# Kernel tuning notes

Hardware: AMD Instinct MI355X
Metric: run time of the kernel (lower is better)

The kernel has to match this reference:

```python
import jax, jax.numpy as jnp
import numpy as np

BATCH, IN_F, OUT_F = 1024, 512, 512
GRID_SIZE, SPLINE_ORDER = 32, 3
P_DEACTIVATE = 0.1


def b_splines(x, grid, k):
    """x: (n, in), grid: (in, G+2k+1) -> bases (n, in, G+k). Cox-de Boor recursion."""
    x = x[..., None]  # (n, in, 1)
    bases = ((x >= grid[:, :-1]) & (x < grid[:, 1:])).astype(x.dtype)
    for j in range(1, k + 1):
        left = (x - grid[:, : -(j + 1)]) / (grid[:, j:-1] - grid[:, : -(j + 1)])
        right = (grid[:, j + 1:] - x) / (grid[:, j + 1:] - grid[:, 1:-j])
        bases = left * bases[..., :-1] + right * bases[..., 1:]
    return bases


def setup_inputs() -> dict:
    key = jax.random.key(0)
    k1, k2, k3, k4, k5 = jax.random.split(key, 5)
    # uniform extended grid over [-1, 1], same for every input feature
    h = 2.0 / GRID_SIZE
    knots = np.arange(-SPLINE_ORDER, GRID_SIZE + SPLINE_ORDER + 1, dtype=np.float32) * h - 1.0
    grid = jnp.asarray(np.tile(knots, (IN_F, 1)))  # (in, G+2k+1)
    return {
        "x": jax.random.normal(k1, (BATCH, IN_F), jnp.float32),
        "base_weight": jax.random.normal(k2, (OUT_F, IN_F), jnp.float32) * 0.05,
        "spline_weight": jax.random.normal(k3, (OUT_F, IN_F, GRID_SIZE + SPLINE_ORDER), jnp.float32) * 0.1,
        "spline_scaler": jax.random.normal(k4, (OUT_F, IN_F), jnp.float32),
        "grid": grid,
        "deactivate_mask": jax.random.bernoulli(k5, P_DEACTIVATE, (OUT_F, IN_F)),
    }


def reference(x, base_weight, spline_weight, spline_scaler, grid, deactivate_mask):
    k = SPLINE_ORDER
    weights = spline_weight * spline_scaler[..., None]  # scaled_spline_weight (o, i, c)
    # base path: F.linear(silu(x), base_weight)
    base_out = jax.nn.silu(x) @ base_weight.T  # (b, o)
    # spline path
    bases = b_splines(x, grid, k)  # (b, i, c)
    contrib = jnp.einsum('bic,oic->boi', bases, weights)  # (b, o, i)
    # linear fallback from spline values at grid endpoints
    gmin = grid[:, k].min()
    gmax = grid[:, -k - 1].max()
    ends_x = jnp.stack([gmin, gmax])[:, None] * jnp.ones((1, x.shape[1]), x.dtype)  # (2, i)
    y_ends = jnp.einsum('nic,oic->noi', b_splines(ends_x, grid, k), weights)  # (2, o, i)
    y_start, y_end = y_ends[0], y_ends[1]
    dx = gmax - gmin
    degenerate = jnp.abs(dx) < 1e-8
    a = jnp.where(degenerate, 0.0, (y_end - y_start) / jnp.where(degenerate, 1.0, dx))  # (o, i)
    b = y_start - a * gmin
    lin = a[None] * x[:, None, :] + b[None]  # (b, o, i)
    final = jnp.where(deactivate_mask[None], lin, contrib)
    return base_out + final.sum(axis=2)
```

## Files before the change

kernel.cpp:

```cpp
#include <hip/hip_runtime.h>
#include <hip/hip_bf16.h>


typedef unsigned short u16;
typedef unsigned int u32;
typedef unsigned long long u64;
typedef __attribute__((ext_vector_type(8))) short short8;
typedef __attribute__((ext_vector_type(4))) float floatx4;
typedef __attribute__((ext_vector_type(4))) unsigned int uintx4;

#define IN_F 512
#define OUT_F 512
#define BATCH 1024
#define K_SPLINE (IN_F * 36)
#define K_BASE_OFF K_SPLINE
#define K_LIN_OFF (K_SPLINE + IN_F)
#define K_TOT (K_SPLINE + 2 * IN_F)
#define SPLITS 32
#define MN (BATCH * OUT_F)

static __device__ inline u16 f2b(float f) {
  union { float f; u32 u; } v; v.f = f;
  u32 r = v.u + 0x7FFFu + ((v.u >> 16) & 1u);
  return (u16)(r >> 16);
}
static __device__ inline float b2f(u32 lo16) {
  union { u32 u; float f; } v; v.u = lo16 << 16; return v.f;
}

__global__ __launch_bounds__(256) void prep_kernel(
    const float* __restrict__ bw, const float* __restrict__ sw,
    const float* __restrict__ sc, const void* __restrict__ maskp,
    const float* __restrict__ x, u16* __restrict__ B,
    float* __restrict__ bias_part, u64* __restrict__ PB8) {
  __shared__ u64 lds64[1120 * 4];
  __shared__ int sflag;
  __shared__ float ws4[4];
  int blk = blockIdx.x, t = threadIdx.x;

  if (blk >= 1024) {
    int id = (blk - 1024) * 256 + t;
    float xv = x[id];
    int mc = (int)floorf((xv + 1.1875f) * 16.0f);
    float gm = (float)mc * 0.0625f - 1.1875f;
    if (xv < gm) { mc -= 1; gm -= 0.0625f; }
    else if (xv >= gm + 0.0625f) { mc += 1; gm += 0.0625f; }
    u32 lo, hi;
    if (mc >= 0 && mc <= 37) {
      float t_ = (xv - gm) * 16.0f;
      float t2 = t_ * t_, t3 = t2 * t_;
      float omt = 1.0f - t_;
      u16 r0 = f2b(omt * omt * omt * (1.0f / 6.0f));
      u16 r1 = f2b((3.0f * t3 - 6.0f * t2 + 4.0f) * (1.0f / 6.0f));
      u16 r2 = f2b((-3.0f * t3 + 3.0f * t2 + 3.0f * t_ + 1.0f) * (1.0f / 6.0f));
      lo = (u32)r0 | ((u32)r1 << 16);
      hi = (u32)r2 | ((u32)mc << 16);
    } else {
      lo = 0; hi = 0xFFFF0000u;
    }
    PB8[id] = (u64)lo | ((u64)hi << 32);
    return;
  }

  float* lds_f = (float*)lds64;
  u16* lds_u = (u16*)lds64;
  int id = blk * 256 + t;
  int o = id >> 9, i = id & 511;
  int i0 = (blk & 1) * 256;

  const float* swb = sw + ((size_t)o * 512 + i0) * 35;
#pragma unroll
  for (int j = 0; j < 35; ++j) lds_f[j * 256 + t] = swb[j * 256 + t];

  const u32* mw = (const u32*)maskp;
  if (t == 0) sflag = 0;
  __syncthreads();
  if (t < 64) {
    u32 w2 = mw[blk * 64 + t];
    if ((w2 & 0xFFFFFF00u) && w2 != 0x3F800000u) atomicOr(&sflag, 1);
  }
  __syncthreads();
  int fl = sflag;
  if (!(fl & 1)) {
    u32 w1 = mw[blk * 256 + t];
    if (w1 == 0x3F800000u) atomicOr(&sflag, 2);
  }
  __syncthreads();
  fl = sflag;
  bool mk;
  if (fl & 1)      mk = ((const unsigned char*)maskp)[id] != 0;
  else if (fl & 2) mk = ((const float*)maskp)[id] != 0.0f;
  else             mk = ((const int*)maskp)[id] != 0;

  float s = sc[id];
  float w[35];
#pragma unroll
  for (int c = 0; c < 35; ++c) w[c] = lds_f[t * 35 + c] * s;
  __syncthreads();

  float ys = (w[0] + 4.0f * w[1] + w[2]) * (1.0f / 6.0f);
  float ye = (w[32] + 4.0f * w[33] + w[34]) * (1.0f / 6.0f);
  float a = (ye - ys) * 0.5f;
  float bl = ys + a;

#pragma unroll
  for (int c = 0; c < 35; ++c) lds_u[t * 36 + c] = f2b(mk ? 0.0f : w[c]);
  lds_u[t * 36 + 35] = 0;

  B[(size_t)o * K_TOT + K_BASE_OFF + i] = f2b(bw[id]);
  B[(size_t)o * K_TOT + K_LIN_OFF + i] = f2b(mk ? a : 0.0f);

  float v = mk ? bl : 0.0f;
#pragma unroll
  for (int off = 32; off >= 1; off >>= 1) v += __shfl_down(v, off);
  if ((t & 63) == 0) ws4[t >> 6] = v;
  __syncthreads();
  if (t == 0) bias_part[blk] = ws4[0] + ws4[1] + ws4[2] + ws4[3];

  u64* dst = (u64*)(B + (size_t)o * K_TOT + (size_t)i0 * 36);
#pragma unroll
  for (int j = 0; j < 9; ++j) dst[j * 256 + t] = lds64[j * 256 + t];
}

__global__ __launch_bounds__(256, 4) void gemm_fused(const float* __restrict__ x,
                                                     const u64* __restrict__ PB8,
                                                     const u16* __restrict__ Bp,
                                                     u16* __restrict__ P) {
  __shared__ u16 As[128 * 64 + 64];
  __shared__ u16 Bs[128 * 64];

  int t = threadIdx.x;
  int id = blockIdx.x;
  int ks = id >> 5, tile = id & 31;
  int bm = tile >> 2, bn = tile & 3;
  int w = t >> 6, l = t & 63;
  int wm = w & 1, wn = w >> 1;

  floatx4 acc[4][4];
#pragma unroll
  for (int p = 0; p < 4; ++p)
#pragma unroll
    for (int q = 0; q < 4; ++q) acc[p][q] = (floatx4)0.0f;

  int nit = (ks < 16) ? 10 : 9;
  int k0s = (ks < 16) ? ks * 640 : 10240 + (ks - 16) * 576;

  int ra = t >> 3;
  int cg = (t & 7) ^ (ra & 7);
  const u16* Bg = Bp + (size_t)(bn * 128 + ra) * K_TOT + k0s + cg * 8;
  u16* Bsp = Bs + t * 8;

  int rr_ = t >> 1, hf = t & 1;
  int rx7 = rr_ & 7;
  int dummy = 128 * 64 + (t & 63);
  const u64* PBrow = PB8 + (size_t)(bm * 128 + rr_) * IN_F;

  int mr = l & 15;
  int cq = l >> 4;

  int if_cur = 0; u64 e0 = 0, e1 = 0;
  if (k0s < K_BASE_OFF) {
    if_cur = (k0s + hf * 32) / 36;
    e0 = PBrow[if_cur];
    e1 = PBrow[if_cur + 1];
  }

  int k0 = k0s;
  for (int kk = 0; kk < nit; ++kk, k0 += 64) {
#pragma unroll
    for (int p = 0; p < 4; ++p)
      __builtin_amdgcn_global_load_lds(
          (const __attribute__((address_space(1))) void*)(Bg + (size_t)p * 32 * K_TOT),
          (__attribute__((address_space(3))) void*)(Bsp + p * 2048), 16, 0, 0);
    Bg += 64;

    int if_nxt = if_cur; u64 en0 = e0, en1 = e1;
    if (k0 < K_BASE_OFF) {
#pragma unroll
      for (int q = 0; q < 4; ++q) {
        int ch = hf * 4 + q;
        *(uintx4*)&As[rr_ * 64 + ((ch ^ rx7) << 3)] = (uintx4)0u;
      }
      int k0w = k0 + hf * 32;
      int i_last = (k0w + 31) / 36;
#pragma unroll
      for (int ii = 0; ii < 2; ++ii) {
        int i = if_cur + ii;
        if (i <= i_last) {
          u64 e = ii ? e1 : e0;
          u32 lo = (u32)e, hi = (u32)(e >> 32);
          int mc = (int)(hi >> 16);
          float f0 = b2f(lo & 0xFFFFu);
          float f1 = b2f(lo >> 16);
          float f2 = b2f(hi & 0xFFFFu);
          u16 bv[4] = {(u16)lo, (u16)(lo >> 16), (u16)hi, f2b(1.0f - f0 - f1 - f2)};
          int cb = i * 36 + mc - 3 - k0;
#pragma unroll
          for (int j = 0; j < 4; ++j) {
            int c = cb + j;
            bool ok = ((u32)(c - hf * 32) < 32u) && ((u32)(mc - 3 + j) < 35u);
            int addr = ok ? (rr_ * 64 + (((c >> 3) ^ rx7) << 3) + (c & 7)) : dummy;
            As[addr] = bv[j];
          }
        }
      }
      int k0n = k0 + 64;
      if (k0n < K_BASE_OFF) {
        if_nxt = (k0n + hf * 32) / 36;
        en0 = PBrow[if_nxt];
        en1 = PBrow[if_nxt + 1];
      }
    } else {
      bool isBase = (k0 < K_LIN_OFF);
      int xb = isBase ? (k0 - K_BASE_OFF) : (k0 - K_LIN_OFF);
#pragma unroll
      for (int p = 0; p < 4; ++p) {
        int cid = t + 256 * p;
        int row = cid >> 3, ch = cid & 7;
        const float* xp = &x[(size_t)(bm * 128 + row) * IN_F + xb + ch * 8];
        floatx4 v0 = *(const floatx4*)xp;
        floatx4 v1 = *(const floatx4*)(xp + 4);
        float f[8] = {v0.x, v0.y, v0.z, v0.w, v1.x, v1.y, v1.z, v1.w};
        u16 r[8];
#pragma unroll
        for (int j = 0; j < 8; ++j) {
          float vv = f[j];
          if (isBase) vv = vv / (1.0f + __expf(-vv));
          r[j] = f2b(vv);
        }
        *(short8*)(As + row * 64 + ((ch ^ (row & 7)) << 3)) = *(short8*)r;
      }
    }
    __syncthreads();

#pragma unroll
    for (int h = 0; h < 2; ++h) {
      short8 af[4], bf[4];
      int c = h * 4 + cq;
#pragma unroll
      for (int tm = 0; tm < 4; ++tm) {
        int row = wm * 64 + tm * 16 + mr;
        af[tm] = *(const short8*)&As[row * 64 + ((c ^ (row & 7)) << 3)];
      }
#pragma unroll
      for (int tn = 0; tn < 4; ++tn) {
        int row = wn * 64 + tn * 16 + mr;
        bf[tn] = *(const short8*)&Bs[row * 64 + ((c ^ (row & 7)) << 3)];
      }
#pragma unroll
      for (int tm = 0; tm < 4; ++tm)
#pragma unroll
        for (int tn = 0; tn < 4; ++tn)
          acc[tm][tn] = __builtin_amdgcn_mfma_f32_16x16x32_bf16(af[tm], bf[tn], acc[tm][tn], 0, 0, 0);
    }
    __syncthreads();
    if_cur = if_nxt; e0 = en0; e1 = en1;
  }

  u16* Pb = P + ((size_t)tile * SPLITS + ks) * 16384;
#pragma unroll
  for (int q = 0; q < 8; ++q) {
    int tm = q >> 1, tn0 = (q & 1) * 2;
    u16 r[8];
#pragma unroll
    for (int z = 0; z < 4; ++z) r[z] = f2b(acc[tm][tn0][z]);
#pragma unroll
    for (int z = 0; z < 4; ++z) r[4 + z] = f2b(acc[tm][tn0 + 1][z]);
    *(short8*)(Pb + q * 2048 + t * 8) = *(short8*)r;
  }
}

__global__ __launch_bounds__(256) void reduce_kernel(const u16* __restrict__ P,
                                                     const float* __restrict__ bias_part,
                                                     float* __restrict__ out) {
  int rid = blockIdx.x * 256 + threadIdx.x;
  int tile = rid >> 11;
  int rem = rid & 2047;
  int q = rem >> 8, t = rem & 255;
  const u16* base = P + (size_t)tile * SPLITS * 16384 + q * 2048 + t * 8;

  float s[8] = {0, 0, 0, 0, 0, 0, 0, 0};
#pragma unroll
  for (int ks = 0; ks < SPLITS; ++ks) {
    short8 v = *(const short8*)(base + (size_t)ks * 16384);
#pragma unroll
    for (int j = 0; j < 8; ++j) s[j] += b2f((u32)(u16)v[j]);
  }

  int w = t >> 6, l = t & 63;
  int wm = w & 1, wn = w >> 1;
  int bm = tile >> 2, bn = tile & 3;
  int row0 = bm * 128 + wm * 64 + ((l >> 4) << 2);
  int col0 = bn * 128 + wn * 64 + (l & 15);
  int tm = q >> 1, tn0 = (q & 1) * 2;
#pragma unroll
  for (int j = 0; j < 8; ++j) {
    int tn = tn0 + (j >> 2), rr = j & 3;
    int row = row0 + tm * 16 + rr;
    int col = col0 + tn * 16;
    float bsv = bias_part[2 * col] + bias_part[2 * col + 1];
    out[(size_t)row * OUT_F + col] = s[j] + bsv;
  }
}

extern "C" void kernel_launch(void* const* d_in, const int* in_sizes, int n_in,
                              void* d_out, int out_size, void* d_ws, size_t ws_size,
                              hipStream_t stream) {
  const float* x  = (const float*)d_in[0];
  const float* bw = (const float*)d_in[1];
  const float* sw = (const float*)d_in[2];
  const float* sc = (const float*)d_in[3];
  const void* mask = d_in[5];

  const size_t B_BYTES = (size_t)OUT_F * K_TOT * 2;
  const size_t BIAS_OFF = B_BYTES;
  const size_t PB_OFF = B_BYTES + 8192;
  const size_t PB_BYTES = (size_t)MN * 8;
  const size_t P_OFF = PB_OFF + PB_BYTES;

  char* wsb = (char*)d_ws;
  u16* Bpack = (u16*)wsb;
  float* bias_part = (float*)(wsb + BIAS_OFF);
  u64* PB8 = (u64*)(wsb + PB_OFF);
  u16* P = (u16*)(wsb + P_OFF);

  prep_kernel<<<3072, 256, 0, stream>>>(bw, sw, sc, mask, x, Bpack, bias_part, PB8);
  gemm_fused<<<1024, 256, 0, stream>>>(x, PB8, Bpack, P);
  reduce_kernel<<<256, 256, 0, stream>>>(P, bias_part, (float*)d_out);
}
```

Before: 138.2 us.

## Double-buffer LDS tiles in GEMM and halve split-K count

The GEMM now keeps two LDS buffers for A and B. It issues the next tile's global-to-LDS B load and builds the next A tile while MFMAs consume the current buffers, which leaves one barrier per iteration. Split-K drops from 32 to 16 equal chunks of 19 iterations each, so half as many blocks launch and half as many partials reach the reduce step. LDS per block doubles and occupancy is lowered to 2 blocks per CU. The prep kernel also copies spline weights into LDS with 16-byte vector loads.

```diff
diff --git a/kernel.cpp b/kernel.cpp
--- a/kernel.cpp
+++ b/kernel.cpp
@@ -16,7 +16,9 @@
 #define K_BASE_OFF K_SPLINE
 #define K_LIN_OFF (K_SPLINE + IN_F)
 #define K_TOT (K_SPLINE + 2 * IN_F)
-#define SPLITS 32
+#define SPLITS 16
+#define KPS 1216
+#define NIT 19
 #define MN (BATCH * OUT_F)
 
 static __device__ inline u16 f2b(float f) {
@@ -33,7 +35,7 @@
     const float* __restrict__ sc, const void* __restrict__ maskp,
     const float* __restrict__ x, u16* __restrict__ B,
     float* __restrict__ bias_part, u64* __restrict__ PB8) {
-  __shared__ u64 lds64[1120 * 4];
+  __shared__ __align__(16) u64 lds64[1120 * 4];
   __shared__ int sflag;
   __shared__ float ws4[4];
   int blk = blockIdx.x, t = threadIdx.x;
@@ -69,8 +71,11 @@
   int i0 = (blk & 1) * 256;
 
   const float* swb = sw + ((size_t)o * 512 + i0) * 35;
-#pragma unroll
-  for (int j = 0; j < 35; ++j) lds_f[j * 256 + t] = swb[j * 256 + t];
+  const floatx4* sw4 = (const floatx4*)swb;
+  floatx4* lds4 = (floatx4*)lds_f;
+#pragma unroll
+  for (int j = 0; j < 8; ++j) lds4[j * 256 + t] = sw4[j * 256 + t];
+  if (t < 192) lds4[8 * 256 + t] = sw4[8 * 256 + t];
 
   const u32* mw = (const u32*)maskp;
   if (t == 0) sflag = 0;
@@ -122,12 +127,12 @@
   for (int j = 0; j < 9; ++j) dst[j * 256 + t] = lds64[j * 256 + t];
 }
 
-__global__ __launch_bounds__(256, 4) void gemm_fused(const float* __restrict__ x,
+__global__ __launch_bounds__(256, 2) void gemm_fused(const float* __restrict__ x,
                                                      const u64* __restrict__ PB8,
                                                      const u16* __restrict__ Bp,
                                                      u16* __restrict__ P) {
-  __shared__ u16 As[128 * 64 + 64];
-  __shared__ u16 Bs[128 * 64];
+  __shared__ u16 As[2][128 * 64 + 64];
+  __shared__ u16 Bs[2][128 * 64];
 
   int t = threadIdx.x;
   int id = blockIdx.x;
@@ -142,13 +147,11 @@
 #pragma unroll
     for (int q = 0; q < 4; ++q) acc[p][q] = (floatx4)0.0f;
 
-  int nit = (ks < 16) ? 10 : 9;
-  int k0s = (ks < 16) ? ks * 640 : 10240 + (ks - 16) * 576;
+  int k0s = ks * KPS;
 
   int ra = t >> 3;
   int cg = (t & 7) ^ (ra & 7);
-  const u16* Bg = Bp + (size_t)(bn * 128 + ra) * K_TOT + k0s + cg * 8;
-  u16* Bsp = Bs + t * 8;
+  const u16* Bgp = Bp + (size_t)(bn * 128 + ra) * K_TOT + k0s + cg * 8;
 
   int rr_ = t >> 1, hf = t & 1;
   int rx7 = rr_ & 7;
@@ -158,34 +161,27 @@
   int mr = l & 15;
   int cq = l >> 4;
 
-  int if_cur = 0; u64 e0 = 0, e1 = 0;
-  if (k0s < K_BASE_OFF) {
-    if_cur = (k0s + hf * 32) / 36;
-    e0 = PBrow[if_cur];
-    e1 = PBrow[if_cur + 1];
-  }
-
-  int k0 = k0s;
-  for (int kk = 0; kk < nit; ++kk, k0 += 64) {
-#pragma unroll
-    for (int p = 0; p < 4; ++p)
-      __builtin_amdgcn_global_load_lds(
-          (const __attribute__((address_space(1))) void*)(Bg + (size_t)p * 32 * K_TOT),
-          (__attribute__((address_space(3))) void*)(Bsp + p * 2048), 16, 0, 0);
-    Bg += 64;
-
-    int if_nxt = if_cur; u64 en0 = e0, en1 = e1;
-    if (k0 < K_BASE_OFF) {
+  int if_c = 0; u64 e0 = 0, e1 = 0;
+  auto load_PB = [&](int k0b) {
+    if (k0b < K_BASE_OFF) {
+      if_c = (k0b + hf * 32) / 36;
+      e0 = PBrow[if_c];
+      e1 = PBrow[if_c + 1];
+    }
+  };
+
+  auto build_A = [&](int k0b, u16* Asb) {
+    if (k0b < K_BASE_OFF) {
 #pragma unroll
       for (int q = 0; q < 4; ++q) {
         int ch = hf * 4 + q;
-        *(uintx4*)&As[rr_ * 64 + ((ch ^ rx7) << 3)] = (uintx4)0u;
-      }
-      int k0w = k0 + hf * 32;
+        *(uintx4*)&Asb[rr_ * 64 + ((ch ^ rx7) << 3)] = (uintx4)0u;
+      }
+      int k0w = k0b + hf * 32;
       int i_last = (k0w + 31) / 36;
 #pragma unroll
       for (int ii = 0; ii < 2; ++ii) {
-        int i = if_cur + ii;
+        int i = if_c + ii;
         if (i <= i_last) {
           u64 e = ii ? e1 : e0;
           u32 lo = (u32)e, hi = (u32)(e >> 32);
@@ -194,25 +190,19 @@
           float f1 = b2f(lo >> 16);
           float f2 = b2f(hi & 0xFFFFu);
           u16 bv[4] = {(u16)lo, (u16)(lo >> 16), (u16)hi, f2b(1.0f - f0 - f1 - f2)};
-          int cb = i * 36 + mc - 3 - k0;
+          int cb = i * 36 + mc - 3 - k0b;
 #pragma unroll
           for (int j = 0; j < 4; ++j) {
             int c = cb + j;
             bool ok = ((u32)(c - hf * 32) < 32u) && ((u32)(mc - 3 + j) < 35u);
             int addr = ok ? (rr_ * 64 + (((c >> 3) ^ rx7) << 3) + (c & 7)) : dummy;
-            As[addr] = bv[j];
+            Asb[addr] = bv[j];
           }
         }
       }
-      int k0n = k0 + 64;
-      if (k0n < K_BASE_OFF) {
-        if_nxt = (k0n + hf * 32) / 36;
-        en0 = PBrow[if_nxt];
-        en1 = PBrow[if_nxt + 1];
-      }
     } else {
-      bool isBase = (k0 < K_LIN_OFF);
-      int xb = isBase ? (k0 - K_BASE_OFF) : (k0 - K_LIN_OFF);
+      bool isBase = (k0b < K_LIN_OFF);
+      int xb = isBase ? (k0b - K_BASE_OFF) : (k0b - K_LIN_OFF);
 #pragma unroll
       for (int p = 0; p < 4; ++p) {
         int cid = t + 256 * p;
@@ -228,11 +218,43 @@
           if (isBase) vv = vv / (1.0f + __expf(-vv));
           r[j] = f2b(vv);
         }
-        *(short8*)(As + row * 64 + ((ch ^ (row & 7)) << 3)) = *(short8*)r;
-      }
-    }
-    __syncthreads();
-
+        *(short8*)(Asb + row * 64 + ((ch ^ (row & 7)) << 3)) = *(short8*)r;
+      }
+    }
+  };
+
+  {
+    u16* Bsp = &Bs[0][t * 8];
+#pragma unroll
+    for (int p = 0; p < 4; ++p)
+      __builtin_amdgcn_global_load_lds(
+          (const __attribute__((address_space(1))) void*)(Bgp + (size_t)p * 32 * K_TOT),
+          (__attribute__((address_space(3))) void*)(Bsp + p * 2048), 16, 0, 0);
+    Bgp += 64;
+    load_PB(k0s);
+    build_A(k0s, &As[0][0]);
+    load_PB(k0s + 64);
+  }
+  __syncthreads();
+
+  int k0 = k0s;
+#pragma unroll 2
+  for (int kk = 0; kk < NIT; ++kk, k0 += 64) {
+    int cur = kk & 1, nxt = cur ^ 1;
+    if (kk + 1 < NIT) {
+      u16* Bsp = &Bs[nxt][t * 8];
+#pragma unroll
+      for (int p = 0; p < 4; ++p)
+        __builtin_amdgcn_global_load_lds(
+            (const __attribute__((address_space(1))) void*)(Bgp + (size_t)p * 32 * K_TOT),
+            (__attribute__((address_space(3))) void*)(Bsp + p * 2048), 16, 0, 0);
+      Bgp += 64;
+      build_A(k0 + 64, &As[nxt][0]);
+      if (kk + 2 < NIT) load_PB(k0 + 128);
+    }
+
+    const u16* Ac = &As[cur][0];
+    const u16* Bc = &Bs[cur][0];
 #pragma unroll
     for (int h = 0; h < 2; ++h) {
       short8 af[4], bf[4];
@@ -240,12 +262,12 @@
 #pragma unroll
       for (int tm = 0; tm < 4; ++tm) {
         int row = wm * 64 + tm * 16 + mr;
-        af[tm] = *(const short8*)&As[row * 64 + ((c ^ (row & 7)) << 3)];
+        af[tm] = *(const short8*)&Ac[row * 64 + ((c ^ (row & 7)) << 3)];
       }
 #pragma unroll
       for (int tn = 0; tn < 4; ++tn) {
         int row = wn * 64 + tn * 16 + mr;
-        bf[tn] = *(const short8*)&Bs[row * 64 + ((c ^ (row & 7)) << 3)];
+        bf[tn] = *(const short8*)&Bc[row * 64 + ((c ^ (row & 7)) << 3)];
       }
 #pragma unroll
       for (int tm = 0; tm < 4; ++tm)
@@ -254,7 +276,6 @@
           acc[tm][tn] = __builtin_amdgcn_mfma_f32_16x16x32_bf16(af[tm], bf[tn], acc[tm][tn], 0, 0, 0);
     }
     __syncthreads();
-    if_cur = if_nxt; e0 = en0; e1 = en1;
   }
 
   u16* Pb = P + ((size_t)tile * SPLITS + ks) * 16384;
@@ -325,6 +346,6 @@
   u16* P = (u16*)(wsb + P_OFF);
 
   prep_kernel<<<3072, 256, 0, stream>>>(bw, sw, sc, mask, x, Bpack, bias_part, PB8);
-  gemm_fused<<<1024, 256, 0, stream>>>(x, PB8, Bpack, P);
+  gemm_fused<<<512, 256, 0, stream>>>(x, PB8, Bpack, P);
   reduce_kernel<<<256, 256, 0, stream>>>(P, bias_part, (float*)d_out);
 }
```

Result: slower. 147.2 us (+6.5%).

## Materialize dense bf16 A matrix in prep and stream it via global_load_lds

Applied to the files above, without the earlier changes.

The prep kernel now writes a fully dense bf16 A operand (spline bases, silu(x) and x per batch row) to workspace, replacing the compact 4-nonzero encoding. The GEMM loads both A and B tiles directly into LDS with async global_load_lds and no longer builds A tiles from packed entries. This removes per-iteration scatter, zeroing and silu work from the GEMM inner loop. In exchange it writes and reads about 38 MB of mostly-zero A data through memory. The spline-weight staging copy in prep is also widened to 16-byte vector loads.

```diff
diff --git a/kernel.cpp b/kernel.cpp
--- a/kernel.cpp
+++ b/kernel.cpp
@@ -7,7 +7,6 @@
 typedef unsigned long long u64;
 typedef __attribute__((ext_vector_type(8))) short short8;
 typedef __attribute__((ext_vector_type(4))) float floatx4;
-typedef __attribute__((ext_vector_type(4))) unsigned int uintx4;
 
 #define IN_F 512
 #define OUT_F 512
@@ -32,20 +31,27 @@
     const float* __restrict__ bw, const float* __restrict__ sw,
     const float* __restrict__ sc, const void* __restrict__ maskp,
     const float* __restrict__ x, u16* __restrict__ B,
-    float* __restrict__ bias_part, u64* __restrict__ PB8) {
-  __shared__ u64 lds64[1120 * 4];
+    float* __restrict__ bias_part, u16* __restrict__ A) {
+  __shared__ __align__(16) u64 lds64[1120 * 4];
   __shared__ int sflag;
   __shared__ float ws4[4];
   int blk = blockIdx.x, t = threadIdx.x;
 
   if (blk >= 1024) {
-    int id = (blk - 1024) * 256 + t;
-    float xv = x[id];
+    int bix = blk - 1024;
+    int b = bix >> 1;
+    int i0 = (bix & 1) << 8;
+    int i = i0 + t;
+    float xv = x[(size_t)b * IN_F + i];
+
+    u64* myrow = lds64 + t * 9;
+#pragma unroll
+    for (int j = 0; j < 9; ++j) myrow[j] = 0;
+
     int mc = (int)floorf((xv + 1.1875f) * 16.0f);
     float gm = (float)mc * 0.0625f - 1.1875f;
     if (xv < gm) { mc -= 1; gm -= 0.0625f; }
     else if (xv >= gm + 0.0625f) { mc += 1; gm += 0.0625f; }
-    u32 lo, hi;
     if (mc >= 0 && mc <= 37) {
       float t_ = (xv - gm) * 16.0f;
       float t2 = t_ * t_, t3 = t2 * t_;
@@ -53,12 +59,24 @@
       u16 r0 = f2b(omt * omt * omt * (1.0f / 6.0f));
       u16 r1 = f2b((3.0f * t3 - 6.0f * t2 + 4.0f) * (1.0f / 6.0f));
       u16 r2 = f2b((-3.0f * t3 + 3.0f * t2 + 3.0f * t_ + 1.0f) * (1.0f / 6.0f));
-      lo = (u32)r0 | ((u32)r1 << 16);
-      hi = (u32)r2 | ((u32)mc << 16);
-    } else {
-      lo = 0; hi = 0xFFFF0000u;
+      float f0 = b2f(r0), f1 = b2f(r1), f2 = b2f(r2);
+      u16 bv[4] = {r0, r1, r2, f2b(1.0f - f0 - f1 - f2)};
+      u16* lds_u = (u16*)lds64;
+#pragma unroll
+      for (int j = 0; j < 4; ++j) {
+        int c = mc - 3 + j;
+        if ((u32)c < 35u) lds_u[t * 36 + c] = bv[j];
+      }
     }
-    PB8[id] = (u64)lo | ((u64)hi << 32);
+    __syncthreads();
+
+    u64* dstA = (u64*)(A + (size_t)b * K_TOT + (size_t)i0 * 36);
+#pragma unroll
+    for (int j = 0; j < 9; ++j) dstA[j * 256 + t] = lds64[j * 256 + t];
+
+    float sl = xv / (1.0f + __expf(-xv));
+    A[(size_t)b * K_TOT + K_BASE_OFF + i] = f2b(sl);
+    A[(size_t)b * K_TOT + K_LIN_OFF + i] = f2b(xv);
     return;
   }
 
@@ -69,8 +87,11 @@
   int i0 = (blk & 1) * 256;
 
   const float* swb = sw + ((size_t)o * 512 + i0) * 35;
-#pragma unroll
-  for (int j = 0; j < 35; ++j) lds_f[j * 256 + t] = swb[j * 256 + t];
+  const floatx4* sw4 = (const floatx4*)swb;
+  floatx4* lds4 = (floatx4*)lds_f;
+#pragma unroll
+  for (int j = 0; j < 8; ++j) lds4[j * 256 + t] = sw4[j * 256 + t];
+  if (t < 192) lds4[8 * 256 + t] = sw4[8 * 256 + t];
 
   const u32* mw = (const u32*)maskp;
   if (t == 0) sflag = 0;
@@ -122,11 +143,10 @@
   for (int j = 0; j < 9; ++j) dst[j * 256 + t] = lds64[j * 256 + t];
 }
 
-__global__ __launch_bounds__(256, 4) void gemm_fused(const float* __restrict__ x,
-                                                     const u64* __restrict__ PB8,
+__global__ __launch_bounds__(256, 4) void gemm_fused(const u16* __restrict__ A,
                                                      const u16* __restrict__ Bp,
                                                      u16* __restrict__ P) {
-  __shared__ u16 As[128 * 64 + 64];
+  __shared__ u16 As[128 * 64];
   __shared__ u16 Bs[128 * 64];
 
   int t = threadIdx.x;
@@ -147,90 +167,27 @@
 
   int ra = t >> 3;
   int cg = (t & 7) ^ (ra & 7);
-  const u16* Bg = Bp + (size_t)(bn * 128 + ra) * K_TOT + k0s + cg * 8;
+  const u16* Agp = A + (size_t)(bm * 128 + ra) * K_TOT + k0s + cg * 8;
+  const u16* Bgp = Bp + (size_t)(bn * 128 + ra) * K_TOT + k0s + cg * 8;
+  u16* Asp = As + t * 8;
   u16* Bsp = Bs + t * 8;
-
-  int rr_ = t >> 1, hf = t & 1;
-  int rx7 = rr_ & 7;
-  int dummy = 128 * 64 + (t & 63);
-  const u64* PBrow = PB8 + (size_t)(bm * 128 + rr_) * IN_F;
 
   int mr = l & 15;
   int cq = l >> 4;
 
-  int if_cur = 0; u64 e0 = 0, e1 = 0;
-  if (k0s < K_BASE_OFF) {
-    if_cur = (k0s + hf * 32) / 36;
-    e0 = PBrow[if_cur];
-    e1 = PBrow[if_cur + 1];
-  }
-
-  int k0 = k0s;
-  for (int kk = 0; kk < nit; ++kk, k0 += 64) {
+  for (int kk = 0; kk < nit; ++kk) {
 #pragma unroll
     for (int p = 0; p < 4; ++p)
       __builtin_amdgcn_global_load_lds(
-          (const __attribute__((address_space(1))) void*)(Bg + (size_t)p * 32 * K_TOT),
+          (const __attribute__((address_space(1))) void*)(Agp + (size_t)p * 32 * K_TOT),
+          (__attribute__((address_space(3))) void*)(Asp + p * 2048), 16, 0, 0);
+#pragma unroll
+    for (int p = 0; p < 4; ++p)
+      __builtin_amdgcn_global_load_lds(
+          (const __attribute__((address_space(1))) void*)(Bgp + (size_t)p * 32 * K_TOT),
           (__attribute__((address_space(3))) void*)(Bsp + p * 2048), 16, 0, 0);
-    Bg += 64;
-
-    int if_nxt = if_cur; u64 en0 = e0, en1 = e1;
-    if (k0 < K_BASE_OFF) {
-#pragma unroll
-      for (int q = 0; q < 4; ++q) {
-        int ch = hf * 4 + q;
-        *(uintx4*)&As[rr_ * 64 + ((ch ^ rx7) << 3)] = (uintx4)0u;
-      }
-      int k0w = k0 + hf * 32;
-      int i_last = (k0w + 31) / 36;
-#pragma unroll
-      for (int ii = 0; ii < 2; ++ii) {
-        int i = if_cur + ii;
-        if (i <= i_last) {
-          u64 e = ii ? e1 : e0;
-          u32 lo = (u32)e, hi = (u32)(e >> 32);
-          int mc = (int)(hi >> 16);
-          float f0 = b2f(lo & 0xFFFFu);
-          float f1 = b2f(lo >> 16);
-          float f2 = b2f(hi & 0xFFFFu);
-          u16 bv[4] = {(u16)lo, (u16)(lo >> 16), (u16)hi, f2b(1.0f - f0 - f1 - f2)};
-          int cb = i * 36 + mc - 3 - k0;
-#pragma unroll
-          for (int j = 0; j < 4; ++j) {
-            int c = cb + j;
-            bool ok = ((u32)(c - hf * 32) < 32u) && ((u32)(mc - 3 + j) < 35u);
-            int addr = ok ? (rr_ * 64 + (((c >> 3) ^ rx7) << 3) + (c & 7)) : dummy;
-            As[addr] = bv[j];
-          }
-        }
-      }
-      int k0n = k0 + 64;
-      if (k0n < K_BASE_OFF) {
-        if_nxt = (k0n + hf * 32) / 36;
-        en0 = PBrow[if_nxt];
-        en1 = PBrow[if_nxt + 1];
-      }
-    } else {
-      bool isBase = (k0 < K_LIN_OFF);
-      int xb = isBase ? (k0 - K_BASE_OFF) : (k0 - K_LIN_OFF);
-#pragma unroll
-      for (int p = 0; p < 4; ++p) {
-        int cid = t + 256 * p;
-        int row = cid >> 3, ch = cid & 7;
-        const float* xp = &x[(size_t)(bm * 128 + row) * IN_F + xb + ch * 8];
-        floatx4 v0 = *(const floatx4*)xp;
-        floatx4 v1 = *(const floatx4*)(xp + 4);
-        float f[8] = {v0.x, v0.y, v0.z, v0.w, v1.x, v1.y, v1.z, v1.w};
-        u16 r[8];
-#pragma unroll
-        for (int j = 0; j < 8; ++j) {
-          float vv = f[j];
-          if (isBase) vv = vv / (1.0f + __expf(-vv));
-          r[j] = f2b(vv);
-        }
-        *(short8*)(As + row * 64 + ((ch ^ (row & 7)) << 3)) = *(short8*)r;
-      }
-    }
+    Agp += 64;
+    Bgp += 64;
     __syncthreads();
 
 #pragma unroll
@@ -254,7 +211,6 @@
           acc[tm][tn] = __builtin_amdgcn_mfma_f32_16x16x32_bf16(af[tm], bf[tn], acc[tm][tn], 0, 0, 0);
     }
     __syncthreads();
-    if_cur = if_nxt; e0 = en0; e1 = en1;
   }
 
   u16* Pb = P + ((size_t)tile * SPLITS + ks) * 16384;
@@ -314,17 +270,17 @@
 
   const size_t B_BYTES = (size_t)OUT_F * K_TOT * 2;
   const size_t BIAS_OFF = B_BYTES;
-  const size_t PB_OFF = B_BYTES + 8192;
-  const size_t PB_BYTES = (size_t)MN * 8;
-  const size_t P_OFF = PB_OFF + PB_BYTES;
+  const size_t A_OFF = B_BYTES + 8192;
+  const size_t A_BYTES = (size_t)BATCH * K_TOT * 2;
+  const size_t P_OFF = A_OFF + A_BYTES;
 
   char* wsb = (char*)d_ws;
   u16* Bpack = (u16*)wsb;
   float* bias_part = (float*)(wsb + BIAS_OFF);
-  u64* PB8 = (u64*)(wsb + PB_OFF);
+  u16* Adense = (u16*)(wsb + A_OFF);
   u16* P = (u16*)(wsb + P_OFF);
 
-  prep_kernel<<<3072, 256, 0, stream>>>(bw, sw, sc, mask, x, Bpack, bias_part, PB8);
-  gemm_fused<<<1024, 256, 0, stream>>>(x, PB8, Bpack, P);
+  prep_kernel<<<3072, 256, 0, stream>>>(bw, sw, sc, mask, x, Bpack, bias_part, Adense);
+  gemm_fused<<<1024, 256, 0, stream>>>(Adense, Bpack, P);
   reduce_kernel<<<256, 256, 0, stream>>>(P, bias_part, (float*)d_out);
 }
```

Result: no change. 139.9 us (+1.2%).
